# Performance work log

Measured on AMD Instinct MI355X. Metric: run time of the kernel, lower is better.

The kernel has to match this reference:

```python
import jax, jax.numpy as jnp
import numpy as np

B, L, D, H, K = 4, 4096, 1024, 16, 256

def setup_inputs() -> dict:
    key = jax.random.key(0)
    ks = jax.random.split(key, 11)
    s = 0.02
    return {
        "x": jax.random.normal(ks[0], (B, L, D), jnp.float32),
        "Wq": jax.random.normal(ks[1], (D, D), jnp.float32) * s,
        "bq": jax.random.normal(ks[2], (D,), jnp.float32) * s,
        "Wk": jax.random.normal(ks[3], (D, D), jnp.float32) * s,
        "bk": jax.random.normal(ks[4], (D,), jnp.float32) * s,
        "Wv": jax.random.normal(ks[5], (D, D), jnp.float32) * s,
        "bv": jax.random.normal(ks[6], (D,), jnp.float32) * s,
        "E": jax.random.normal(ks[7], (L, K), jnp.float32),
        "F": jax.random.normal(ks[8], (L, K), jnp.float32),
        "Wo": jax.random.normal(ks[9], (D, D), jnp.float32) * s,
        "bo": jax.random.normal(ks[10], (D,), jnp.float32) * s,
        "n_heads": H,
    }

def reference(x, Wq, bq, Wk, bk, Wv, bv, E, F, Wo, bo, n_heads):
    Bc, Lc, Dc = x.shape
    hd = Dc // n_heads
    scale = hd ** -0.5
    # QKV projections (torch Linear: x @ W.T + b; here W stored as [in,out])
    q = (x @ Wq + bq).reshape(Bc, Lc, n_heads, hd)  # blhd
    k = (x @ Wk + bk).reshape(Bc, Lc, n_heads, hd)
    v = (x @ Wv + bv).reshape(Bc, Lc, n_heads, hd)
    # Low-rank projection of K/V sequence dim: L -> K
    kE = jnp.einsum('blhd,lk->bhkd', k, E[:Lc])
    vF = jnp.einsum('blhd,lk->bhkd', v, F[:Lc])
    # Attention over compressed dim k
    qk = jnp.einsum('blhd,bhkd->bhlk', q, kE) * scale
    attn = jax.nn.softmax(qk, axis=-1)
    out = jnp.einsum('bhlk,bhkd->blhd', attn, vF).reshape(Bc, Lc, Dc)
    return out @ Wo + bo
```

## Files before the change

### kernel.cpp

```cpp
#include <hip/hip_runtime.h>

typedef _Float16 half_t;
typedef __attribute__((ext_vector_type(8))) _Float16 f16x8;
typedef __attribute__((ext_vector_type(4))) _Float16 f16x4;
typedef __attribute__((ext_vector_type(4))) float f32x4;
typedef __attribute__((ext_vector_type(4))) float float4v;

__device__ __forceinline__ void gload_lds16(const void* g, void* l) {
  __builtin_amdgcn_global_load_lds(
      (const __attribute__((address_space(1))) void*)g,
      (__attribute__((address_space(3))) void*)l, 16, 0, 0);
}

template<int OUTF16>
__global__ __launch_bounds__(512, 2)
void gemm_big(const half_t* __restrict__ A, const half_t* __restrict__ Bt,
              void* __restrict__ Cv, const float* __restrict__ bias, float alpha)
{
  __shared__ __attribute__((aligned(16))) char lds[131072];
  const int tid = threadIdx.x, w = tid >> 6, lane = tid & 63;
  const int wr = w >> 2, wc = w & 3;
  const int g = lane >> 4, cc = lane & 15;
  const int m0 = blockIdx.x * 256, n0 = blockIdx.y * 256;

  const int sr = tid >> 2, ss = tid & 3;
  const int swz = (ss ^ ((sr >> 1) & 3)) << 3;
  const long aoff = (long)(m0 + sr) * 1024 + swz;
  const long boff = (long)(n0 + sr) * 1024 + swz;
  const int dst = tid * 16;

  char* b0 = lds;
  char* b1 = lds + 32768;
  char* b2 = lds + 65536;
  char* b3 = lds + 98304;

  const f32x4 zero = {0.f, 0.f, 0.f, 0.f};
  f32x4 acc[8][4];
#pragma unroll
  for (int i = 0; i < 8; ++i)
#pragma unroll
    for (int j = 0; j < 4; ++j) acc[i][j] = zero;

  auto STAGE = [&](int tau, char* bp) {
    const half_t* Ak = A + tau * 32;
    const half_t* Bk = Bt + tau * 32;
    gload_lds16(Ak + aoff,          bp + dst);
    gload_lds16(Ak + aoff + 131072, bp + 8192 + dst);
    gload_lds16(Bk + boff,          bp + 16384 + dst);
    gload_lds16(Bk + boff + 131072, bp + 24576 + dst);
  };

  STAGE(0, b0);
  STAGE(1, b1);
  STAGE(2, b2);
  asm volatile("s_waitcnt vmcnt(8)" ::: "memory");
  __builtin_amdgcn_s_barrier();
  __builtin_amdgcn_sched_barrier(0);

  const int aslot = (g ^ ((cc >> 1) & 3)) << 4;
  const int arow = wr * 128 + cc;
  const int brow = wc * 64 + cc;

#pragma unroll 1
  for (int t = 0; t < 32; ++t) {
    if (t < 29) STAGE(t + 3, b3);
    f16x8 af[8], bf[4];
#pragma unroll
    for (int mf = 0; mf < 8; ++mf)
      af[mf] = *(const f16x8*)(b0 + (arow + mf * 16) * 64 + aslot);
#pragma unroll
    for (int nf = 0; nf < 4; ++nf)
      bf[nf] = *(const f16x8*)(b0 + 16384 + (brow + nf * 16) * 64 + aslot);
    __builtin_amdgcn_s_setprio(1);
#pragma unroll
    for (int mf = 0; mf < 8; ++mf)
#pragma unroll
      for (int nf = 0; nf < 4; ++nf)
        acc[mf][nf] = __builtin_amdgcn_mfma_f32_16x16x32_f16(af[mf], bf[nf], acc[mf][nf], 0, 0, 0);
    __builtin_amdgcn_s_setprio(0);
    __builtin_amdgcn_sched_barrier(0);
    if (t == 31) break;
    if (t < 29)       { asm volatile("s_waitcnt vmcnt(8)" ::: "memory"); }
    else if (t == 29) { asm volatile("s_waitcnt vmcnt(4)" ::: "memory"); }
    else              { asm volatile("s_waitcnt vmcnt(0)" ::: "memory"); }
    __builtin_amdgcn_s_barrier();
    __builtin_amdgcn_sched_barrier(0);
    char* tmp = b0; b0 = b1; b1 = b2; b2 = b3; b3 = tmp;
  }

#pragma unroll
  for (int mf = 0; mf < 8; ++mf)
#pragma unroll
    for (int nf = 0; nf < 4; ++nf)
#pragma unroll
      for (int r = 0; r < 4; ++r) {
        const int row = m0 + wr * 128 + mf * 16 + g * 4 + r;
        const int col = n0 + wc * 64 + nf * 16 + cc;
        float v = (acc[mf][nf][r] + bias[col]) * alpha;
        if (OUTF16) ((half_t*)Cv)[(long)row * 1024 + col] = (half_t)v;
        else        ((float*)Cv)[(long)row * 1024 + col] = v;
      }
}

template<int BM, int BN, int WM, int WN, int OUTF16, int MODE, int SK>
__global__ __launch_bounds__(256, 2)
void gemm_bt(const half_t* __restrict__ A, const half_t* __restrict__ Bt,
             void* __restrict__ Cv, const float* __restrict__ bias,
             const float* __restrict__ rowscale,
             int M, int N, int K, int lda, int ldb, int ldc, float alpha,
             long sA, long sB, long sC)
{
  constexpr int FM = WM / 16, FN = WN / 16, CW = BN / WN;
  __shared__ __attribute__((aligned(16))) half_t As[BM * 32];
  __shared__ __attribute__((aligned(16))) half_t Bs[BN * 32];

  const int tid = threadIdx.x, w = tid >> 6, lane = tid & 63;
  const int wr = w / CW, wc = w % CW;
  const int z = blockIdx.z / SK, ks = blockIdx.z % SK;
  const half_t* Ab = A + (long)z * sA;
  const half_t* Bb = Bt + (long)z * sB;
  const int m0 = blockIdx.x * BM, n0 = blockIdx.y * BN;
  const int g = lane >> 4, cc = lane & 15;
  const int srow = lane >> 2, scol = (lane & 3) * 8;

  const f32x4 zero = {0.f, 0.f, 0.f, 0.f};
  f32x4 acc[FM][FN];
#pragma unroll
  for (int i = 0; i < FM; ++i)
#pragma unroll
    for (int j = 0; j < FN; ++j) acc[i][j] = zero;

  const int kchunk = K / SK;
  for (int kt = ks * kchunk; kt < (ks + 1) * kchunk; kt += 32) {
#pragma unroll
    for (int j = 0; j < BM / 64; ++j) {
      const int bi = w * (BM / 64) + j;
      gload_lds16(Ab + (long)(m0 + bi * 16 + srow) * lda + kt + scol, &As[bi * 512]);
    }
#pragma unroll
    for (int j = 0; j < BN / 64; ++j) {
      const int bi = w * (BN / 64) + j;
      gload_lds16(Bb + (long)(n0 + bi * 16 + srow) * ldb + kt + scol, &Bs[bi * 512]);
    }
    __syncthreads();

    f16x8 af[FM], bf[FN];
#pragma unroll
    for (int i = 0; i < FM; ++i)
      af[i] = *(const f16x8*)&As[(wr * WM + i * 16 + cc) * 32 + g * 8];
#pragma unroll
    for (int j = 0; j < FN; ++j)
      bf[j] = *(const f16x8*)&Bs[(wc * WN + j * 16 + cc) * 32 + g * 8];
#pragma unroll
    for (int i = 0; i < FM; ++i)
#pragma unroll
      for (int j = 0; j < FN; ++j)
        acc[i][j] = __builtin_amdgcn_mfma_f32_16x16x32_f16(af[i], bf[j], acc[i][j], 0, 0, 0);
    __syncthreads();
  }

  const long coff = (long)z * sC;
#pragma unroll
  for (int i = 0; i < FM; ++i)
#pragma unroll
    for (int j = 0; j < FN; ++j)
#pragma unroll
      for (int r = 0; r < 4; ++r) {
        const int row = m0 + wr * WM + i * 16 + g * 4 + r;
        const int col = n0 + wc * WN + j * 16 + cc;
        float v = acc[i][j][r];
        if (MODE == 1) v = (v + bias[col]) * alpha;
        if (MODE == 2 || MODE == 4) v = v + rowscale[row] * bias[col];
        if (MODE == 3) {
          const int nb = gridDim.z / SK;
          ((float*)Cv)[((long)ks * nb + z) * sC + (long)row * ldc + col] = v;
        } else if (MODE == 4) {
          ((half_t*)Cv)[coff + (long)(col >> 6) * ((long)M * 64) + (long)row * 64 + (col & 63)]
              = (half_t)v;
        } else {
          if (OUTF16) ((half_t*)Cv)[coff + (long)row * ldc + col] = (half_t)v;
          else        ((float*)Cv)[coff + (long)row * ldc + col] = v;
        }
      }
}

__global__ __launch_bounds__(512, 2)
void attn_fused(const half_t* __restrict__ q, const half_t* __restrict__ kEh,
                const half_t* __restrict__ vFt, half_t* __restrict__ outp, int L)
{
  __shared__ __attribute__((aligned(16))) half_t Ks[256 * 64];
  __shared__ __attribute__((aligned(16))) half_t Vs[64 * 256];
  const int tid = threadIdx.x, w = tid >> 6, lane = tid & 63;
  const int g = lane >> 4, c = lane & 15;
  const int l0 = blockIdx.x * 256, h = blockIdx.y, b = blockIdx.z;

  const half_t* keh = kEh + (long)(b * 16 + h) * 16384;
  const half_t* vfh = vFt + (long)b * 262144 + (long)h * 16384;
  const half_t* qb  = q + ((long)b * L + l0 + w * 32) * 1024 + h * 64;
  half_t* ob = outp + ((long)b * L + l0 + w * 32) * 1024 + h * 64;

#pragma unroll
  for (int i = 0; i < 4; ++i) {
    const int row = i * 64 + (tid >> 3), slot = tid & 7;
    gload_lds16(keh + row * 64 + ((slot ^ (row & 7)) << 3),
                (char*)Ks + i * 8192 + tid * 16);
  }
#pragma unroll
  for (int i = 0; i < 4; ++i) {
    const int row = i * 16 + (tid >> 5), slot = tid & 31;
    gload_lds16(vfh + row * 256 + ((slot ^ (row & 7)) << 3),
                (char*)Vs + i * 8192 + tid * 16);
  }

  f16x8 qf[2][2];
#pragma unroll
  for (int fi = 0; fi < 2; ++fi)
#pragma unroll
    for (int ks = 0; ks < 2; ++ks)
      qf[fi][ks] = *(const f16x8*)(qb + (long)(fi * 16 + c) * 1024 + ks * 32 + g * 8);

  __syncthreads();

  const f32x4 zero = {0.f, 0.f, 0.f, 0.f};
  f32x4 o[2][4];
#pragma unroll
  for (int fi = 0; fi < 2; ++fi)
#pragma unroll
    for (int fd = 0; fd < 4; ++fd) o[fi][fd] = zero;
  float mrun[2] = {-3.0e38f, -3.0e38f};
  float lrun[2] = {0.f, 0.f};

  for (int ch = 0; ch < 4; ++ch) {
    f32x4 s[2][4];
#pragma unroll
    for (int fi = 0; fi < 2; ++fi)
#pragma unroll
      for (int fj = 0; fj < 4; ++fj) s[fi][fj] = zero;
#pragma unroll
    for (int fj = 0; fj < 4; ++fj) {
      const int krow = ch * 64 + fj * 16 + c;
      const char* kb = (const char*)Ks + krow * 128;
      f16x8 k0 = *(const f16x8*)(kb + ((g ^ (c & 7)) << 4));
      f16x8 k1 = *(const f16x8*)(kb + (((4 + g) ^ (c & 7)) << 4));
#pragma unroll
      for (int fi = 0; fi < 2; ++fi) {
        s[fi][fj] = __builtin_amdgcn_mfma_f32_16x16x32_f16(k0, qf[fi][0], s[fi][fj], 0, 0, 0);
        s[fi][fj] = __builtin_amdgcn_mfma_f32_16x16x32_f16(k1, qf[fi][1], s[fi][fj], 0, 0, 0);
      }
    }

    f16x4 p[2][4];
#pragma unroll
    for (int fi = 0; fi < 2; ++fi) {
      float cm = -3.0e38f;
#pragma unroll
      for (int fj = 0; fj < 4; ++fj)
#pragma unroll
        for (int r = 0; r < 4; ++r) cm = fmaxf(cm, s[fi][fj][r]);
      cm = fmaxf(cm, __shfl_xor(cm, 16));
      cm = fmaxf(cm, __shfl_xor(cm, 32));
      const float mnew = fmaxf(mrun[fi], cm);
      const float sc = __expf(mrun[fi] - mnew);
      float csum = 0.f;
#pragma unroll
      for (int fj = 0; fj < 4; ++fj) {
        f16x4 fr;
#pragma unroll
        for (int r = 0; r < 4; ++r) {
          float e = __expf(s[fi][fj][r] - mnew);
          fr[r] = (half_t)e; csum += e;
        }
        p[fi][fj] = fr;
      }
      csum += __shfl_xor(csum, 16);
      csum += __shfl_xor(csum, 32);
      lrun[fi] = lrun[fi] * sc + csum;
      mrun[fi] = mnew;
#pragma unroll
      for (int fd = 0; fd < 4; ++fd)
#pragma unroll
        for (int r = 0; r < 4; ++r) o[fi][fd][r] *= sc;
    }

#pragma unroll
    for (int kc = 0; kc < 4; ++kc) {
      const int s16 = ch * 8 + kc * 2 + (g >> 1);
      f16x4 va[4];
#pragma unroll
      for (int fd = 0; fd < 4; ++fd) {
        const int drow = fd * 16 + c;
        va[fd] = *(const f16x4*)((const char*)Vs + drow * 512 +
                                 ((s16 ^ (c & 7)) << 4) + (g & 1) * 8);
      }
#pragma unroll
      for (int fi = 0; fi < 2; ++fi)
#pragma unroll
        for (int fd = 0; fd < 4; ++fd)
          o[fi][fd] = __builtin_amdgcn_mfma_f32_16x16x16f16(va[fd], p[fi][kc], o[fi][fd], 0, 0, 0);
    }
  }

#pragma unroll
  for (int fi = 0; fi < 2; ++fi) {
    const float inv = 1.0f / lrun[fi];
#pragma unroll
    for (int fd = 0; fd < 4; ++fd) {
      f16x4 st;
#pragma unroll
      for (int r = 0; r < 4; ++r) st[r] = (half_t)(o[fi][fd][r] * inv);
      *(f16x4*)(ob + (long)(fi * 16 + c) * 1024 + fd * 16 + g * 4) = st;
    }
  }
}

__global__ void reduce4_f16(const float* __restrict__ in, half_t* __restrict__ out) {
  long i = ((long)blockIdx.x * 256 + threadIdx.x) * 4;
  float4v a = *(const float4v*)(in + i);
#pragma unroll
  for (int ks = 1; ks < 4; ++ks) {
    float4v t = *(const float4v*)(in + (long)ks * 2097152 + i);
    a.x += t.x; a.y += t.y; a.z += t.z; a.w += t.w;
  }
  f16x4 o;
  o[0] = (half_t)a.x; o[1] = (half_t)a.y; o[2] = (half_t)a.z; o[3] = (half_t)a.w;
  *(f16x4*)(out + i) = o;
}

__global__ void xpass(const float* __restrict__ x, half_t* __restrict__ xhf,
                      half_t* __restrict__ xT) {
  __shared__ float t[32][33];
  const int b = blockIdx.z, d0 = blockIdx.x * 32, l0 = blockIdx.y * 32;
  const int tx = threadIdx.x, ty = threadIdx.y;
  const float* ip = x + ((long)b * 4096 + l0) * 1024 + d0;
  half_t* oh = xhf + ((long)b * 4096 + l0) * 1024 + d0;
#pragma unroll
  for (int j = 0; j < 4; ++j) {
    float v = ip[(long)(ty + 8 * j) * 1024 + tx];
    t[ty + 8 * j][tx] = v;
    oh[(long)(ty + 8 * j) * 1024 + tx] = (half_t)v;
  }
  __syncthreads();
  half_t* ot = xT + ((long)b * 1024 + d0) * 4096 + l0;
#pragma unroll
  for (int j = 0; j < 4; ++j)
    ot[(long)(ty + 8 * j) * 4096 + tx] = (half_t)t[tx][ty + 8 * j];
}

__global__ void efpass(const float* __restrict__ in, half_t* __restrict__ outT,
                       float* __restrict__ ssum) {
  __shared__ float t[32][33];
  __shared__ float ps[8][32];
  const int k0 = blockIdx.x * 32, l0 = blockIdx.y * 32;
  const int tx = threadIdx.x, ty = threadIdx.y;
  float p = 0.f;
#pragma unroll
  for (int j = 0; j < 4; ++j) {
    float v = in[(long)(l0 + ty + 8 * j) * 256 + k0 + tx];
    t[ty + 8 * j][tx] = v; p += v;
  }
  ps[ty][tx] = p;
  __syncthreads();
  if (ty == 0) {
    float a = 0.f;
#pragma unroll
    for (int r = 0; r < 8; ++r) a += ps[r][tx];
    atomicAdd(&ssum[k0 + tx], a);
  }
#pragma unroll
  for (int j = 0; j < 4; ++j)
    outT[(long)(k0 + ty + 8 * j) * 4096 + l0 + tx] = (half_t)t[tx][ty + 8 * j];
}

__global__ void transpose_f32_f16(const float* __restrict__ in, half_t* __restrict__ out,
                                  int R, int C) {
  __shared__ float t[32][33];
  const int cx = blockIdx.x * 32 + threadIdx.x;
  const int r0 = blockIdx.y * 32;
#pragma unroll
  for (int j = 0; j < 4; ++j)
    t[threadIdx.y + 8 * j][threadIdx.x] = in[(long)(r0 + threadIdx.y + 8 * j) * C + cx];
  __syncthreads();
  const int rx = r0 + threadIdx.x;
  const int cy = blockIdx.x * 32 + threadIdx.y;
#pragma unroll
  for (int j = 0; j < 4; ++j)
    out[(long)(cy + 8 * j) * R + rx] = (half_t)t[threadIdx.x][threadIdx.y + 8 * j];
}

extern "C" void kernel_launch(void* const* d_in, const int* in_sizes, int n_in,
                              void* d_out, int out_size, void* d_ws, size_t ws_size,
                              hipStream_t stream)
{
  const float* x  = (const float*)d_in[0];
  const float* Wq = (const float*)d_in[1];
  const float* bq = (const float*)d_in[2];
  const float* Wk = (const float*)d_in[3];
  const float* bk = (const float*)d_in[4];
  const float* Wv = (const float*)d_in[5];
  const float* bv = (const float*)d_in[6];
  const float* E  = (const float*)d_in[7];
  const float* F  = (const float*)d_in[8];
  const float* Wo = (const float*)d_in[9];
  const float* bo = (const float*)d_in[10];
  float* out = (float*)d_out;

  char* ws = (char*)d_ws;
  half_t* xhf  = (half_t*)(ws);
  half_t* xT   = (half_t*)(ws + 33554432);
  half_t* qhf  = (half_t*)(ws + 67108864);
  half_t* Wqt  = (half_t*)(ws + 100663296);
  half_t* Wkt  = Wqt + 1048576;
  half_t* Wvt  = Wkt + 1048576;
  half_t* Wot  = Wvt + 1048576;
  half_t* EFt  = (half_t*)(ws + 109051904);
  half_t* xEF  = (half_t*)(ws + 113246208);
  half_t* kEb  = (half_t*)(ws + 117440512);
  half_t* vFtb = (half_t*)(ws + 119537664);
  float*  sEF  = (float*)(ws + 121634816);
  half_t* outp = xhf;
  float*  xEFf = (float*)d_out;

  hipMemsetAsync(sEF, 0, 2048, stream);
  dim3 tb(32, 8);
  xpass<<<dim3(32, 128, 4), tb, 0, stream>>>(x, xhf, xT);
  efpass<<<dim3(8, 128, 1), tb, 0, stream>>>(E, EFt, sEF);
  efpass<<<dim3(8, 128, 1), tb, 0, stream>>>(F, EFt + 1048576, sEF + 256);
  transpose_f32_f16<<<dim3(32, 32, 1), tb, 0, stream>>>(Wq, Wqt, 1024, 1024);
  transpose_f32_f16<<<dim3(32, 32, 1), tb, 0, stream>>>(Wk, Wkt, 1024, 1024);
  transpose_f32_f16<<<dim3(32, 32, 1), tb, 0, stream>>>(Wv, Wvt, 1024, 1024);
  transpose_f32_f16<<<dim3(32, 32, 1), tb, 0, stream>>>(Wo, Wot, 1024, 1024);

  gemm_bt<128,128,64,64,0,3,4><<<dim3(4, 8, 16), 256, 0, stream>>>(
      EFt, xT, (void*)xEFf, nullptr, nullptr, 512, 1024, 4096, 4096, 4096, 1024, 1.f,
      0, 4194304, 524288);
  reduce4_f16<<<2048, 256, 0, stream>>>(xEFf, xEF);

  gemm_big<1><<<dim3(64, 4), 512, 0, stream>>>(xhf, Wqt, qhf, bq, 0.125f);
  gemm_bt<128,128,64,64,1,4,1><<<dim3(2, 8, 4), 256, 0, stream>>>(
      xEF, Wkt, kEb, bk, sEF, 256, 1024, 1024, 1024, 1024, 1024, 1.f,
      524288, 0, 262144);
  gemm_bt<128,128,64,64,1,2,1><<<dim3(8, 2, 4), 256, 0, stream>>>(
      Wvt, xEF + 262144, vFtb, sEF + 256, bv, 1024, 256, 1024, 1024, 1024, 256, 1.f,
      0, 524288, 262144);
  attn_fused<<<dim3(16, 16, 4), 512, 0, stream>>>(qhf, kEb, vFtb, outp, 4096);
  gemm_big<0><<<dim3(64, 4), 512, 0, stream>>>(outp, Wot, (void*)out, bo, 1.0f);
  (void)in_sizes; (void)n_in; (void)out_size; (void)ws_size;
}
```

Measured before the change: 248.1 us.

## Restructure big GEMM mainloop into 8-wave ping-pong with half-tile staging

Replaces the 4-stage K=32 ring buffer in gemm_big with a double-buffered K=64 tile. Each tile is split into four phases that interleave LDS fragment reads, one quarter of the next tile's global->LDS loads, and a 4x4 MFMA block, with a barrier per phase. The goal is finer overlap of memory and compute and half as many outer iterations. The cost is more barriers per tile and shallower prefetch depth, and the hand-tuned vmcnt counts must match the issued loads exactly.

```diff
diff --git a/kernel.cpp b/kernel.cpp
--- a/kernel.cpp
+++ b/kernel.cpp
@@ -23,16 +23,9 @@
   const int g = lane >> 4, cc = lane & 15;
   const int m0 = blockIdx.x * 256, n0 = blockIdx.y * 256;
 
-  const int sr = tid >> 2, ss = tid & 3;
-  const int swz = (ss ^ ((sr >> 1) & 3)) << 3;
-  const long aoff = (long)(m0 + sr) * 1024 + swz;
-  const long boff = (long)(n0 + sr) * 1024 + swz;
-  const int dst = tid * 16;
-
-  char* b0 = lds;
-  char* b1 = lds + 32768;
-  char* b2 = lds + 65536;
-  char* b3 = lds + 98304;
+  const int srow2 = tid >> 2, sslot = tid & 3;
+  const int swslot = sslot ^ ((srow2 >> 1) & 3);
+  const int swr = (g ^ ((cc >> 1) & 3)) << 4;
 
   const f32x4 zero = {0.f, 0.f, 0.f, 0.f};
   f32x4 acc[8][4];
@@ -41,51 +34,65 @@
 #pragma unroll
     for (int j = 0; j < 4; ++j) acc[i][j] = zero;
 
-  auto STAGE = [&](int tau, char* bp) {
-    const half_t* Ak = A + tau * 32;
-    const half_t* Bk = Bt + tau * 32;
-    gload_lds16(Ak + aoff,          bp + dst);
-    gload_lds16(Ak + aoff + 131072, bp + 8192 + dst);
-    gload_lds16(Bk + boff,          bp + 16384 + dst);
-    gload_lds16(Bk + boff + 131072, bp + 24576 + dst);
+  auto STAGE_HALF = [&](int ktile, int hh, char* sb) {
+    const int kk = hh >> 1, isB = hh & 1;
+    const half_t* src = isB ? Bt : A;
+    const int base_row = isB ? n0 : m0;
+    const long rowoff = (long)(base_row + srow2) * 1024 + ktile * 64 + kk * 32 + swslot * 8;
+    char* d = sb + isB * 32768 + kk * 16384;
+    gload_lds16(src + rowoff,          d + tid * 16);
+    gload_lds16(src + rowoff + 131072, d + 8192 + tid * 16);
   };
 
-  STAGE(0, b0);
-  STAGE(1, b1);
-  STAGE(2, b2);
-  asm volatile("s_waitcnt vmcnt(8)" ::: "memory");
+  {
+    char* b0 = lds;
+    STAGE_HALF(0, 0, b0); STAGE_HALF(0, 1, b0);
+    STAGE_HALF(0, 2, b0); STAGE_HALF(0, 3, b0);
+  }
+  asm volatile("s_waitcnt vmcnt(4)" ::: "memory");
   __builtin_amdgcn_s_barrier();
-  __builtin_amdgcn_sched_barrier(0);
-
-  const int aslot = (g ^ ((cc >> 1) & 3)) << 4;
-  const int arow = wr * 128 + cc;
-  const int brow = wc * 64 + cc;
 
 #pragma unroll 1
-  for (int t = 0; t < 32; ++t) {
-    if (t < 29) STAGE(t + 3, b3);
-    f16x8 af[8], bf[4];
-#pragma unroll
-    for (int mf = 0; mf < 8; ++mf)
-      af[mf] = *(const f16x8*)(b0 + (arow + mf * 16) * 64 + aslot);
-#pragma unroll
-    for (int nf = 0; nf < 4; ++nf)
-      bf[nf] = *(const f16x8*)(b0 + 16384 + (brow + nf * 16) * 64 + aslot);
-    __builtin_amdgcn_s_setprio(1);
-#pragma unroll
-    for (int mf = 0; mf < 8; ++mf)
-#pragma unroll
-      for (int nf = 0; nf < 4; ++nf)
-        acc[mf][nf] = __builtin_amdgcn_mfma_f32_16x16x32_f16(af[mf], bf[nf], acc[mf][nf], 0, 0, 0);
-    __builtin_amdgcn_s_setprio(0);
-    __builtin_amdgcn_sched_barrier(0);
-    if (t == 31) break;
-    if (t < 29)       { asm volatile("s_waitcnt vmcnt(8)" ::: "memory"); }
-    else if (t == 29) { asm volatile("s_waitcnt vmcnt(4)" ::: "memory"); }
-    else              { asm volatile("s_waitcnt vmcnt(0)" ::: "memory"); }
-    __builtin_amdgcn_s_barrier();
-    __builtin_amdgcn_sched_barrier(0);
-    char* tmp = b0; b0 = b1; b1 = b2; b2 = b3; b3 = tmp;
+  for (int n = 0; n < 16; ++n) {
+    const char* rb = lds + ((n & 1) << 16);
+    char* sb = lds + (((n + 1) & 1) << 16);
+    f16x8 bf[4];
+#pragma unroll
+    for (int ph = 0; ph < 4; ++ph) {
+      const int kk = ph >> 1, fh = ph & 1;
+      f16x8 af[4];
+      const char* Ah = rb + kk * 16384;
+#pragma unroll
+      for (int mf = 0; mf < 4; ++mf)
+        af[mf] = *(const f16x8*)(Ah + (wr * 128 + fh * 64 + mf * 16 + cc) * 64 + swr);
+      if (fh == 0) {
+        const char* Bh = rb + 32768 + kk * 16384;
+#pragma unroll
+        for (int nf = 0; nf < 4; ++nf)
+          bf[nf] = *(const f16x8*)(Bh + (wc * 64 + nf * 16 + cc) * 64 + swr);
+      }
+      if (n < 15) STAGE_HALF(n + 1, ph, sb);
+      __builtin_amdgcn_sched_barrier(0);
+      __builtin_amdgcn_s_barrier();
+      asm volatile("s_waitcnt lgkmcnt(0)" ::: "memory");
+      __builtin_amdgcn_sched_barrier(0);
+      __builtin_amdgcn_s_setprio(1);
+#pragma unroll
+      for (int mf = 0; mf < 4; ++mf)
+#pragma unroll
+        for (int nf = 0; nf < 4; ++nf)
+          acc[fh * 4 + mf][nf] =
+              __builtin_amdgcn_mfma_f32_16x16x32_f16(af[mf], bf[nf], acc[fh * 4 + mf][nf], 0, 0, 0);
+      __builtin_amdgcn_s_setprio(0);
+      __builtin_amdgcn_sched_barrier(0);
+      if (ph == 1) {
+        if (n < 15) { asm volatile("s_waitcnt vmcnt(4)" ::: "memory"); }
+        else        { asm volatile("s_waitcnt vmcnt(0)" ::: "memory"); }
+      } else if (ph == 3) {
+        if (n < 15) { asm volatile("s_waitcnt vmcnt(4)" ::: "memory"); }
+      }
+      __builtin_amdgcn_s_barrier();
+    }
   }
 
 #pragma unroll
```

Result: no change. 250.5 us (+1.0%).
